# Performance work log

Hardware: AMD Instinct MI355X
Metric: run time of the kernel (lower is better)

The kernel has to match this reference:

```python
import jax, jax.numpy as jnp
import numpy as np

EPS = 1e-15


def _cdist(a, b):
    # batched euclidean pairwise distance, a:[B,N,K] b:[B,M,K] -> [B,N,M]
    d2 = (jnp.sum(a * a, -1)[:, :, None] + jnp.sum(b * b, -1)[:, None, :]
          - 2.0 * jnp.einsum('bik,bjk->bij', a, b))
    return jnp.sqrt(jnp.maximum(d2, 0.0))


def _rank3_diag(d_flat):
    # [B,N] -> [B,N,N] diagonal
    eye = jnp.eye(d_flat.shape[1], dtype=d_flat.dtype)
    return eye * d_flat[:, :, None]


def _trace(m):
    return jnp.einsum('bjj->b', m)


def dense_ct_rewiring(x, adj, s, mask):
    s = jnp.tanh(s)
    m = mask[:, :, None].astype(x.dtype)
    x = x * m
    s = s * m
    k = s.shape[-1]
    d_flat = jnp.sum(adj, axis=-1)              # [B,N]
    d = _rank3_diag(d_flat) + EPS               # EPS added to full matrix (faithful to torch)
    L = d - adj
    out_adj = jnp.einsum('bnk,bnm,bml->bkl', s, L, s)
    ct_num = _trace(out_adj)
    ct_den = _trace(jnp.einsum('bnk,bnm,bml->bkl', s, d, s)) + EPS
    ct_dist = _cdist(s, s)                      # [B,N,N]
    vol = _trace(d)                             # [B]
    ct_dist = ct_dist / vol[:, None, None]
    adj_new = ct_dist * adj
    ct_loss = jnp.mean(ct_num / ct_den)
    ss = jnp.einsum('bnk,bnl->bkl', s, s)
    i_s = jnp.eye(k, dtype=ss.dtype)
    ss_n = jnp.sqrt(jnp.sum(ss * ss, axis=(-1, -2), keepdims=True))
    diff = ss / ss_n - i_s
    ortho_loss = jnp.sqrt(jnp.sum(diff * diff))  # global Frobenius norm, mean of scalar
    return adj_new, ct_loss, ortho_loss


def dense_mincut_pool(x, adj, s, mask):
    s = jax.nn.softmax(s, axis=-1)
    m = mask[:, :, None].astype(x.dtype)
    x = x * m
    s = s * m
    k = s.shape[-1]
    out = jnp.einsum('bnk,bnf->bkf', s, x)
    out_adj = jnp.einsum('bnk,bnm,bml->bkl', s, adj, s)
    mincut_num = _trace(out_adj)
    d_flat = jnp.sum(adj, axis=-1) + EPS
    d = _rank3_diag(d_flat)
    mincut_den = _trace(jnp.einsum('bnk,bnm,bml->bkl', s, d, s))
    mincut_loss = jnp.mean(-(mincut_num / mincut_den))
    ss = jnp.einsum('bnk,bnl->bkl', s, s)
    i_s = jnp.eye(k, dtype=ss.dtype)
    ss_n = jnp.sqrt(jnp.sum(ss * ss, axis=(-1, -2), keepdims=True))
    diff = ss / ss_n - i_s / jnp.sqrt(jnp.asarray(float(k), ss.dtype))
    ortho_loss = jnp.mean(jnp.sqrt(jnp.sum(diff * diff, axis=(-1, -2))))
    # zero diagonal, then symmetric degree normalization
    out_adj = out_adj * (1.0 - i_s)
    dk = jnp.sqrt(jnp.sum(out_adj, axis=-1) + EPS) + EPS  # [B,k]
    out_adj = out_adj / dk[:, None, :] / dk[:, :, None]
    return out, out_adj, mincut_loss, ortho_loss


def dense_graph_conv(x, adj, w_rel, b_rel, w_root):
    # PyG DenseGraphConv(aggr='add'): lin_rel(adj @ x) + lin_root(x)
    return jnp.matmul(jnp.matmul(adj, x), w_rel) + b_rel + jnp.matmul(x, w_root)


def ctnet_forward(x, adj, mask,
                  W_lin1, b_lin1, W_pool1, b_pool1, W_pool2, b_pool2,
                  Wrel1, brel1, Wroot1, Wrel2, brel2, Wroot2,
                  W_lin2, b_lin2, W_lin3, b_lin3):
    x = jnp.matmul(x, W_lin1) + b_lin1
    s1 = jnp.matmul(x, W_pool1) + b_pool1
    adj, ct_loss, ortho1 = dense_ct_rewiring(x, adj, s1, mask)
    x = dense_graph_conv(x, adj, Wrel1, brel1, Wroot1)
    s2 = jnp.matmul(x, W_pool2) + b_pool2
    x, adj, mincut2, ortho2 = dense_mincut_pool(x, adj, s2, mask)
    x = dense_graph_conv(x, adj, Wrel2, brel2, Wroot2)
    x = jnp.sum(x, axis=1)
    x = jax.nn.relu(jnp.matmul(x, W_lin2) + b_lin2)
    x = jnp.matmul(x, W_lin3) + b_lin3
    return jax.nn.log_softmax(x, axis=-1), ct_loss + ortho1, mincut2 + ortho2


def _init_lin(key, fan_in, fan_out):
    k1, k2 = jax.random.split(key)
    lim = 1.0 / np.sqrt(fan_in)
    W = jax.random.uniform(k1, (fan_in, fan_out), jnp.float32, -lim, lim)
    b = jax.random.uniform(k2, (fan_out,), jnp.float32, -lim, lim)
    return W, b


def setup_inputs() -> dict:
    key = jax.random.key(0)
    ks = jax.random.split(key, 12)
    B, N, Fin, H, K, OUT, K2 = 16, 1024, 128, 32, 64, 10, 16
    x = jax.random.normal(ks[0], (B, N, Fin), jnp.float32)
    adj = jax.random.uniform(ks[1], (B, N, N), jnp.float32)
    mask = jnp.ones((B, N), jnp.bool_)
    W_lin1, b_lin1 = _init_lin(ks[2], Fin, H)
    W_pool1, b_pool1 = _init_lin(ks[3], H, K)
    W_pool2, b_pool2 = _init_lin(ks[4], H, K2)
    Wrel1, brel1 = _init_lin(ks[5], H, H)
    Wroot1, _ = _init_lin(ks[6], H, H)
    Wrel2, brel2 = _init_lin(ks[7], H, H)
    Wroot2, _ = _init_lin(ks[8], H, H)
    W_lin2, b_lin2 = _init_lin(ks[9], H, H)
    W_lin3, b_lin3 = _init_lin(ks[10], H, OUT)
    return dict(x=x, adj=adj, mask=mask,
                W_lin1=W_lin1, b_lin1=b_lin1, W_pool1=W_pool1, b_pool1=b_pool1,
                W_pool2=W_pool2, b_pool2=b_pool2,
                Wrel1=Wrel1, brel1=brel1, Wroot1=Wroot1,
                Wrel2=Wrel2, brel2=brel2, Wroot2=Wroot2,
                W_lin2=W_lin2, b_lin2=b_lin2, W_lin3=W_lin3, b_lin3=b_lin3)


def reference(x, adj, mask,
              W_lin1, b_lin1, W_pool1, b_pool1, W_pool2, b_pool2,
              Wrel1, brel1, Wroot1, Wrel2, brel2, Wroot2,
              W_lin2, b_lin2, W_lin3, b_lin3):
    return ctnet_forward(x, adj, mask,
                         W_lin1, b_lin1, W_pool1, b_pool1, W_pool2, b_pool2,
                         Wrel1, brel1, Wroot1, Wrel2, brel2, Wroot2,
                         W_lin2, b_lin2, W_lin3, b_lin3)
```

## Files before the change

kernel.cpp:

```cpp
#include <hip/hip_runtime.h>

typedef unsigned short u16;
typedef unsigned int   u32;
typedef __attribute__((ext_vector_type(8))) short bf16x8;
typedef __attribute__((ext_vector_type(4))) float f32x4;

#define EPSF 1e-15f

__device__ __forceinline__ float* accp(float* xb, int b, int a) {
    return xb + (size_t)(b*1024 + a/14)*128 + 114 + (a % 14);
}

__device__ __forceinline__ float bf2f(u16 u) {
    union { u32 i; float f; } v; v.i = ((u32)u) << 16; return v.f;
}
__device__ __forceinline__ u16 f2bf(float f) {
    union { u32 i; float f; } v; v.f = f;
    u32 r = v.i + 0x7fffu + ((v.i >> 16) & 1u);
    return (u16)(r >> 16);
}

__global__ __launch_bounds__(256) void k_a(float* xb,
        const float* __restrict__ W1, const float* __restrict__ b1,
        const float* __restrict__ Wp1, const float* __restrict__ bp1)
{
    __shared__ float W1sT[32*133];
    __shared__ float Wp1sT[64*33];
    __shared__ float xs[16][128];
    __shared__ float x1s[16][32];
    int tid = threadIdx.x;
    for (int i = tid; i < 1024; i += 256) {
        int f = i >> 3, c0 = (i & 7)*4;
        float4 v = *(const float4*)&W1[f*32 + c0];
        W1sT[(c0+0)*133 + f] = v.x;
        W1sT[(c0+1)*133 + f] = v.y;
        W1sT[(c0+2)*133 + f] = v.z;
        W1sT[(c0+3)*133 + f] = v.w;
    }
    for (int i = tid; i < 512; i += 256) {
        int h = i >> 4, l0 = (i & 15)*4;
        float4 v = *(const float4*)&Wp1[h*64 + l0];
        Wp1sT[(l0+0)*33 + h] = v.x;
        Wp1sT[(l0+1)*33 + h] = v.y;
        Wp1sT[(l0+2)*33 + h] = v.z;
        Wp1sT[(l0+3)*33 + h] = v.w;
    }
    int rbase = blockIdx.x*16;
    for (int e = tid; e < 512; e += 256) {
        int rr = e >> 5, c = e & 31;
        *(float4*)&xs[rr][c*4] = *(const float4*)&xb[(size_t)(rbase + rr)*128 + c*4];
    }
    __syncthreads();
    int w = tid >> 6, l = tid & 63;
    int col = l & 31, half = l >> 5;
    #pragma unroll
    for (int i = 0; i < 4; ++i) {
        int rr = w*4 + i;
        float* xr = xb + (size_t)(rbase + rr)*128;
        if (l == 33) xr[96] = 0.f;
        if (l < 15) xr[113 + l] = 0.f;
        float acc = half ? 0.f : b1[col];
        const float* xrow = &xs[rr][half*64];
        const float* wrow = &W1sT[col*133 + half*64];
        for (int f = 0; f < 64; ++f) acc += xrow[f]*wrow[f];
        acc += __shfl_down(acc, 32);
        if (l < 32) x1s[rr][l] = acc;
    }
    __syncthreads();
    #pragma unroll
    for (int i = 0; i < 4; ++i) {
        int rr = w*4 + i;
        float* xr = xb + (size_t)(rbase + rr)*128;
        if (l < 32) xr[64 + l] = x1s[rr][l];
        float acc = bp1[l];
        const float* wp = &Wp1sT[l*33];
        for (int h = 0; h < 32; ++h) acc += x1s[rr][h]*wp[h];
        float sv = tanhf(acc);
        u32 me = (u32)f2bf(sv);
        u32 nb = __shfl_down(me, 1);
        if (!(l & 1)) ((u32*)xr)[l >> 1] = me | (nb << 16);
        float svr = bf2f((u16)me);
        float qv = svr*svr;
        for (int off = 32; off; off >>= 1) qv += __shfl_down(qv, off);
        if (l == 0) xr[112] = qv;
    }
}

__global__ __launch_bounds__(256, 5) void k_c(const float* __restrict__ adj, float* xb,
                                              u32* __restrict__ anb)
{
    __shared__ __align__(16) u16 BufA[64*72];
    __shared__ __align__(16) u16 BufB[2][64*72];
    __shared__ __align__(16) float qAs[64], qBs[2][64];
    __shared__ float pw[2][4];
    int tid = threadIdx.x;
    int tjq = blockIdx.x, ti = blockIdx.y, b = blockIdx.z;
    int w = tid >> 6, lane = tid & 63;
    int q = lane >> 4, c16 = lane & 15;
    int rloc = w*16 + c16;
    size_t rowg = (size_t)(b*1024 + ti*64 + rloc);
    float4 a4s[2][4];
    #pragma unroll
    for (int tt = 0; tt < 2; ++tt)
        #pragma unroll
        for (int t = 0; t < 4; ++t)
            a4s[tt][t] = *(const float4*)&adj[rowg*1024 + (tjq*2 + tt)*64 + t*16 + q*4];
    const u32* xu = (const u32*)xb;
    for (int e = tid; e < 512; e += 256) {
        int n = e >> 3, c = e & 7;
        *(float4*)&BufA[n*72 + c*8] = *(const float4*)&xu[(size_t)(b*1024 + ti*64 + n)*128 + c*4];
    }
    for (int e = tid; e < 1024; e += 256) {
        int n2 = e >> 3, c = e & 7;
        int tt = n2 >> 6, n = n2 & 63;
        *(float4*)&BufB[tt][n*72 + c*8] =
            *(const float4*)&xu[(size_t)(b*1024 + (tjq*2 + tt)*64 + n)*128 + c*4];
    }
    if (tid < 64) qAs[tid] = xb[(size_t)(b*1024 + ti*64 + tid)*128 + 112];
    else if (tid < 192) {
        int t2 = tid - 64;
        qBs[t2 >> 6][t2 & 63] =
            xb[(size_t)(b*1024 + (tjq*2 + (t2 >> 6))*64 + (t2 & 63))*128 + 112];
    }
    __syncthreads();
    bf16x8 bfr0 = *(const bf16x8*)&BufA[rloc*72 + q*8];
    bf16x8 bfr1 = *(const bf16x8*)&BufA[rloc*72 + 32 + q*8];
    float qa = qAs[rloc];
    float dsum = 0.f, rsum = 0.f, Pt = 0.f, Qt = 0.f;
    #pragma unroll
    for (int tt = 0; tt < 2; ++tt) {
        f32x4 g[4];
        #pragma unroll
        for (int t = 0; t < 4; ++t) {
            bf16x8 af0 = *(const bf16x8*)&BufB[tt][(t*16 + c16)*72 + q*8];
            bf16x8 af1 = *(const bf16x8*)&BufB[tt][(t*16 + c16)*72 + 32 + q*8];
            f32x4 gg = {0.f, 0.f, 0.f, 0.f};
            gg = __builtin_amdgcn_mfma_f32_16x16x32_bf16(af0, bfr0, gg, 0, 0, 0);
            gg = __builtin_amdgcn_mfma_f32_16x16x32_bf16(af1, bfr1, gg, 0, 0, 0);
            g[t] = gg;
        }
        #pragma unroll
        for (int t = 0; t < 4; ++t) {
            float4 a4 = a4s[tt][t];
            float4 qb4 = *(const float4*)&qBs[tt][t*16 + q*4];
            float av[4] = {a4.x, a4.y, a4.z, a4.w};
            float qb[4] = {qb4.x, qb4.y, qb4.z, qb4.w};
            float o[4];
            #pragma unroll
            for (int rg = 0; rg < 4; ++rg) {
                float d2v = qa + qb[rg] - 2.f*g[t][rg];
                float dist = sqrtf(fmaxf(d2v, 0.f));
                o[rg] = dist * av[rg];
                dsum += av[rg];
                rsum += o[rg];
                Pt += av[rg]*g[t][rg];
                Qt += g[t][rg]*g[t][rg];
            }
            u32 p0 = (u32)f2bf(o[0]) | ((u32)f2bf(o[1]) << 16);
            u32 p1 = (u32)f2bf(o[2]) | ((u32)f2bf(o[3]) << 16);
            *(uint2*)&anb[rowg*512 + (tjq*2 + tt)*32 + t*8 + q*2] = make_uint2(p0, p1);
        }
    }
    rsum += __shfl_xor(rsum, 16); rsum += __shfl_xor(rsum, 32);
    dsum += __shfl_xor(dsum, 16); dsum += __shfl_xor(dsum, 32);
    if (q == 0) {
        atomicAdd(&xb[rowg*128 + 96],  dsum);
        atomicAdd(&xb[rowg*128 + 113], rsum);
    }
    for (int off = 32; off; off >>= 1) { Pt += __shfl_down(Pt, off); Qt += __shfl_down(Qt, off); }
    if (lane == 0) { pw[0][w] = Pt; pw[1][w] = Qt; }
    __syncthreads();
    if (tid == 0) {
        atomicAdd(accp(xb,b,3), pw[0][0]+pw[0][1]+pw[0][2]+pw[0][3]);
        atomicAdd(accp(xb,b,4), pw[1][0]+pw[1][1]+pw[1][2]+pw[1][3]);
    }
}

__global__ __launch_bounds__(256) void k_y(const u32* __restrict__ anb, float* xb)
{
    __shared__ __align__(16) u16 X[16*1032];
    int tid = threadIdx.x;
    int hq = blockIdx.x, ni = blockIdx.y, b = blockIdx.z;
    int w = tid >> 6, lane = tid & 63;
    int q = lane >> 4, c16 = lane & 15;
    int rloc = w*16 + c16;
    size_t rowg = (size_t)(b*1024 + ni*64 + rloc);
    u32* Xu = (u32*)X;
    for (int e = tid; e < 2048; e += 256) {
        int mp = e >> 2, h4 = e & 3;
        int m0 = mp*2;
        const float* p0 = &xb[(size_t)(b*1024 + m0)*128 + 64 + hq*16 + h4*4];
        float4 v0 = *(const float4*)p0;
        float4 v1 = *(const float4*)(p0 + 128);
        Xu[(h4*4 + 0)*516 + mp] = (u32)f2bf(v0.x) | ((u32)f2bf(v1.x) << 16);
        Xu[(h4*4 + 1)*516 + mp] = (u32)f2bf(v0.y) | ((u32)f2bf(v1.y) << 16);
        Xu[(h4*4 + 2)*516 + mp] = (u32)f2bf(v0.z) | ((u32)f2bf(v1.z) << 16);
        Xu[(h4*4 + 3)*516 + mp] = (u32)f2bf(v0.w) | ((u32)f2bf(v1.w) << 16);
    }
    __syncthreads();
    f32x4 acc = {0.f,0.f,0.f,0.f};
    #pragma unroll 8
    for (int ks = 0; ks < 32; ++ks) {
        bf16x8 af = *(const bf16x8*)&anb[rowg*512 + ks*16 + q*4];
        bf16x8 bx = *(const bf16x8*)&X[c16*1032 + ks*32 + q*8];
        acc = __builtin_amdgcn_mfma_f32_16x16x32_bf16(af, bx, acc, 0, 0, 0);
    }
    #pragma unroll
    for (int rg = 0; rg < 4; ++rg) {
        size_t orow = (size_t)(b*1024 + ni*64 + w*16 + q*4 + rg)*128;
        xb[orow + 32 + hq*16 + c16] = acc[rg];
    }
    if (hq == 0 && tid < 64) {
        const float* xr = xb + (size_t)(b*1024 + ni*64 + tid)*128;
        float d = xr[96], qv = xr[112];
        float t0 = d, t1 = d*qv, t2 = qv;
        for (int off = 32; off; off >>= 1) {
            t0 += __shfl_down(t0, off); t1 += __shfl_down(t1, off); t2 += __shfl_down(t2, off);
        }
        if (tid == 0) {
            atomicAdd(accp(xb,b,0), t0);
            atomicAdd(accp(xb,b,1), t1);
            atomicAdd(accp(xb,b,2), t2);
        }
    }
}

__global__ __launch_bounds__(256) void k_d2(float* xb,
        const float* __restrict__ Wrel1, const float* __restrict__ brel1,
        const float* __restrict__ Wroot1,
        const float* __restrict__ Wp2, const float* __restrict__ bp2)
{
    __shared__ float ys[32*34];
    __shared__ float x1n[32*34];
    __shared__ float x2s[32*34];
    __shared__ float s2s[32*17];
    __shared__ float WrT[32*33], WoT[32*33], WpT[16*33];
    __shared__ float pwd[4];
    int tid = threadIdx.x;
    int tq = blockIdx.x, b = blockIdx.y;
    int rbase = b*1024 + tq*32;
    float invv = 1.f / (*accp(xb,b,0) + 1024.f*EPSF);
    {
        int j = tid >> 3, h0 = (tid & 7)*4;
        float4 v = *(const float4*)&Wrel1[j*32 + h0];
        WrT[(h0+0)*33 + j] = v.x;
        WrT[(h0+1)*33 + j] = v.y;
        WrT[(h0+2)*33 + j] = v.z;
        WrT[(h0+3)*33 + j] = v.w;
        float4 v2 = *(const float4*)&Wroot1[j*32 + h0];
        WoT[(h0+0)*33 + j] = v2.x;
        WoT[(h0+1)*33 + j] = v2.y;
        WoT[(h0+2)*33 + j] = v2.z;
        WoT[(h0+3)*33 + j] = v2.w;
    }
    if (tid < 128) {
        int j = tid >> 2, k0 = (tid & 3)*4;
        float4 v = *(const float4*)&Wp2[j*16 + k0];
        WpT[(k0+0)*33 + j] = v.x;
        WpT[(k0+1)*33 + j] = v.y;
        WpT[(k0+2)*33 + j] = v.z;
        WpT[(k0+3)*33 + j] = v.w;
    }
    for (int e = tid; e < 1024; e += 256) {
        int r = e >> 5, h = e & 31;
        const float* xr = xb + (size_t)(rbase + r)*128;
        ys[r*34 + h]  = xr[32 + h] * invv;
        x1n[r*34 + h] = xr[64 + h];
    }
    __syncthreads();
    {
        int h = tid & 31, tg = tid >> 5;
        float brl = brel1[h];
        const float* wr = &WrT[h*33];
        const float* wo = &WoT[h*33];
        #pragma unroll
        for (int i = 0; i < 4; ++i) {
            int r = tg + 8*i;
            float v = brl;
            for (int j = 0; j < 32; ++j)
                v += ys[r*34 + j]*wr[j] + x1n[r*34 + j]*wo[j];
            x2s[r*34 + h] = v;
        }
    }
    __syncthreads();
    {
        int rl = tid & 7, kq = (tid >> 3) & 7, wv = tid >> 6;
        int r = wv*8 + rl;
        int k0 = kq*2;
        float v0 = bp2[k0], v1 = bp2[k0 + 1];
        const float* wp0 = &WpT[k0*33];
        const float* wp1 = &WpT[(k0+1)*33];
        for (int j = 0; j < 32; ++j) {
            float xv = x2s[r*34 + j];
            v0 += xv*wp0[j];
            v1 += xv*wp1[j];
        }
        float mx = fmaxf(v0, v1);
        mx = fmaxf(mx, __shfl_xor(mx, 8));
        mx = fmaxf(mx, __shfl_xor(mx, 16));
        mx = fmaxf(mx, __shfl_xor(mx, 32));
        float e0 = expf(v0 - mx), e1 = expf(v1 - mx);
        float sm = e0 + e1;
        sm += __shfl_xor(sm, 8); sm += __shfl_xor(sm, 16); sm += __shfl_xor(sm, 32);
        float inv = 1.f/sm;
        float sv0 = e0*inv, sv1 = e1*inv;
        s2s[r*17 + k0]     = sv0;
        s2s[r*17 + k0 + 1] = sv1;
        ((u32*)(xb + (size_t)(rbase + r)*128))[kq] =
            (u32)f2bf(sv0) | ((u32)f2bf(sv1) << 16);
        float q2v = sv0*sv0 + sv1*sv1;
        q2v += __shfl_xor(q2v, 8); q2v += __shfl_xor(q2v, 16); q2v += __shfl_xor(q2v, 32);
        float denp = (kq == 0)
            ? (xb[(size_t)(rbase + r)*128 + 113]*invv + EPSF)*q2v : 0.f;
        denp += __shfl_down(denp, 1);
        denp += __shfl_down(denp, 2);
        denp += __shfl_down(denp, 4);
        if ((tid & 63) == 0) pwd[wv] = denp;
    }
    __syncthreads();
    if (tid == 0) atomicAdd(accp(xb,b,5), pwd[0]+pwd[1]+pwd[2]+pwd[3]);
    {
        int k = tid >> 4, l = tid & 15;
        float s = 0.f;
        for (int r = 0; r < 32; ++r) s += s2s[r*17 + k]*s2s[r*17 + l];
        atomicAdd(accp(xb,b,774 + tid), s);
    }
    for (int e = tid; e < 512; e += 256) {
        int k = e >> 5, h = e & 31;
        float s = 0.f;
        for (int r = 0; r < 32; ++r) s += s2s[r*17 + k]*x2s[r*34 + h];
        atomicAdd(accp(xb,b,6 + k*32 + h), s);
    }
}

__global__ __launch_bounds__(256) void k_e(const u32* __restrict__ anb, float* xb)
{
    __shared__ __align__(16) u16 BufS[2][16*72];
    __shared__ __align__(16) u16 BufN[16*72];
    __shared__ __align__(16) u16 zT[16*72];
    int tid = threadIdx.x;
    int miq = blockIdx.x, ni = blockIdx.y, b = blockIdx.z;
    const u32* xu = (const u32*)xb;
    for (int e = tid; e < 512; e += 256) {
        int node = e >> 3, lw = e & 7;
        u32 pp = xu[(size_t)(b*1024 + ni*64 + node)*128 + lw];
        BufN[(lw*2)*72 + node]     = (u16)pp;
        BufN[(lw*2 + 1)*72 + node] = (u16)(pp >> 16);
    }
    for (int e = tid; e < 1024; e += 256) {
        int t = e >> 9, e2 = e & 511;
        int node = e2 >> 3, lw = e2 & 7;
        u32 pp = xu[(size_t)(b*1024 + (miq*2 + t)*64 + node)*128 + lw];
        BufS[t][(lw*2)*72 + node]     = (u16)pp;
        BufS[t][(lw*2 + 1)*72 + node] = (u16)(pp >> 16);
    }
    int w = tid >> 6, lane = tid & 63;
    int q = lane >> 4, c16 = lane & 15;
    int rloc = w*16 + c16;
    size_t arow = (size_t)(b*1024 + ni*64 + rloc)*512;
    bf16x8 ya[2][2];
    #pragma unroll
    for (int t = 0; t < 2; ++t) {
        ya[t][0] = *(const bf16x8*)&anb[arow + (miq*2 + t)*32 + q*4];
        ya[t][1] = *(const bf16x8*)&anb[arow + (miq*2 + t)*32 + 16 + q*4];
    }
    __syncthreads();
    f32x4 zacc = {0.f, 0.f, 0.f, 0.f};
    #pragma unroll
    for (int t = 0; t < 2; ++t) {
        bf16x8 yb0 = *(const bf16x8*)&BufS[t][c16*72 + q*8];
        bf16x8 yb1 = *(const bf16x8*)&BufS[t][c16*72 + 32 + q*8];
        zacc = __builtin_amdgcn_mfma_f32_16x16x32_bf16(ya[t][0], yb0, zacc, 0, 0, 0);
        zacc = __builtin_amdgcn_mfma_f32_16x16x32_bf16(ya[t][1], yb1, zacc, 0, 0, 0);
    }
    #pragma unroll
    for (int rg = 0; rg < 4; ++rg)
        zT[c16*72 + w*16 + q*4 + rg] = f2bf(zacc[rg]);
    __syncthreads();
    if (w == 0) {
        bf16x8 af0 = *(const bf16x8*)&BufN[c16*72 + q*8];
        bf16x8 af1 = *(const bf16x8*)&BufN[c16*72 + 32 + q*8];
        bf16x8 bz0 = *(const bf16x8*)&zT[c16*72 + q*8];
        bf16x8 bz1 = *(const bf16x8*)&zT[c16*72 + 32 + q*8];
        f32x4 oamv = {0.f, 0.f, 0.f, 0.f};
        oamv = __builtin_amdgcn_mfma_f32_16x16x32_bf16(af0, bz0, oamv, 0, 0, 0);
        oamv = __builtin_amdgcn_mfma_f32_16x16x32_bf16(af1, bz1, oamv, 0, 0, 0);
        #pragma unroll
        for (int rg = 0; rg < 4; ++rg)
            atomicAdd(accp(xb, b, 518 + (q*4 + rg)*16 + c16), oamv[rg]);
    }
}

__global__ __launch_bounds__(256) void k_f1(float* xb,
        const float* __restrict__ Wrel2, const float* __restrict__ brel2,
        const float* __restrict__ Wroot2,
        const float* __restrict__ W_lin2, const float* __restrict__ b_lin2,
        const float* __restrict__ W_lin3, const float* __restrict__ b_lin3,
        float* __restrict__ outp)
{
    __shared__ float oam_s[256], ssm_s[256], outm_s[512];
    __shared__ float dks[16], csoa[16];
    __shared__ float cs0[32], cs1[32], xsum[32], x5[32], lgs[10];
    __shared__ float red[4];
    __shared__ int isLast;
    int b = blockIdx.x;
    int tid = threadIdx.x;
    float invv = 1.f / (*accp(xb,b,0) + 1024.f*EPSF);
    oam_s[tid] = *accp(xb,b,518 + tid) * invv;
    ssm_s[tid] = *accp(xb,b,774 + tid);
    for (int e = tid; e < 512; e += 256) outm_s[e] = *accp(xb,b,6 + e);
    __syncthreads();
    if (tid < 16) {
        float rsv = 0.f;
        for (int l = 0; l < 16; ++l) if (l != tid) rsv += oam_s[tid*16 + l];
        dks[tid] = sqrtf(fmaxf(rsv, 0.f) + EPSF) + EPSF;
    }
    {
        float v = ssm_s[tid];
        float p = v*v;
        for (int off = 32; off; off >>= 1) p += __shfl_down(p, off);
        if ((tid & 63) == 0) red[tid >> 6] = p;
    }
    __syncthreads();
    if (tid < 16) {
        float s = 0.f;
        for (int k2 = 0; k2 < 16; ++k2)
            if (k2 != tid) s += oam_s[k2*16 + tid] / dks[k2];
        csoa[tid] = s / dks[tid];
    }
    if (tid < 32) {
        float s0 = 0.f, s1 = 0.f;
        for (int l = 0; l < 16; ++l) {
            float ov = outm_s[l*32 + tid];
            s0 += ov;
            s1 += csoa[l] * ov;
        }
        cs0[tid] = s0; cs1[tid] = s1;
    }
    if (tid == 64) {
        float T1v  = *accp(xb,b,1);
        float Pgv  = *accp(xb,b,3);
        float Q2v  = *accp(xb,b,4);
        float Tq1v = *accp(xb,b,2);
        float T2v  = *accp(xb,b,5);
        float tr2 = 0.f, trs = 0.f;
        for (int k2 = 0; k2 < 16; ++k2) { tr2 += oam_s[k2*17]; trs += ssm_s[k2*17]; }
        float fr2 = red[0] + red[1] + red[2] + red[3];
        __hip_atomic_store(accp(xb,b,1030), (T1v - Pgv) / (T1v + EPSF),
                           __ATOMIC_RELAXED, __HIP_MEMORY_SCOPE_AGENT);
        __hip_atomic_store(accp(xb,b,1031), 65.f - 2.f*Tq1v/sqrtf(fmaxf(Q2v, 1e-30f)),
                           __ATOMIC_RELAXED, __HIP_MEMORY_SCOPE_AGENT);
        __hip_atomic_store(accp(xb,b,1032), -tr2 / T2v,
                           __ATOMIC_RELAXED, __HIP_MEMORY_SCOPE_AGENT);
        __hip_atomic_store(accp(xb,b,1033),
                           sqrtf(fmaxf(2.f - trs/(2.f*sqrtf(fmaxf(fr2, 1e-30f))), 0.f)),
                           __ATOMIC_RELAXED, __HIP_MEMORY_SCOPE_AGENT);
    }
    __syncthreads();
    if (tid < 32) {
        float v = 16.f * brel2[tid];
        for (int j = 0; j < 32; ++j)
            v += cs1[j]*Wrel2[j*32 + tid] + cs0[j]*Wroot2[j*32 + tid];
        xsum[tid] = v;
    }
    __syncthreads();
    if (tid < 32) {
        float v = b_lin2[tid];
        for (int j = 0; j < 32; ++j) v += xsum[j]*W_lin2[j*32 + tid];
        x5[tid] = fmaxf(v, 0.f);
    }
    __syncthreads();
    if (tid < 10) {
        float v = b_lin3[tid];
        for (int j = 0; j < 32; ++j) v += x5[j]*W_lin3[j*10 + tid];
        lgs[tid] = v;
    }
    __syncthreads();
    if (tid < 10) {
        float mx = -1e30f;
        for (int t = 0; t < 10; ++t) mx = fmaxf(mx, lgs[t]);
        float sum = 0.f;
        for (int t = 0; t < 10; ++t) sum += expf(lgs[t] - mx);
        outp[b*10 + tid] = lgs[tid] - mx - logf(sum);
    }
    __syncthreads();
    if (tid == 0) {
        __threadfence();
        float old = atomicAdd(accp(xb,0,1035), 1.f);
        isLast = (old > 14.5f) ? 1 : 0;
    }
    __syncthreads();
    if (isLast && tid < 64) {
        __threadfence();
        int b2 = tid & 15, which = tid >> 4;
        float v = __hip_atomic_load(accp(xb,b2,1030 + which),
                                    __ATOMIC_RELAXED, __HIP_MEMORY_SCOPE_AGENT);
        for (int off = 1; off < 16; off <<= 1) v += __shfl_xor(v, off);
        float ct = __shfl(v, 0);
        float o1 = __shfl(v, 16);
        float mc = __shfl(v, 32);
        float o2 = __shfl(v, 48);
        if (tid == 0) {
            outp[160] = ct/16.f + sqrtf(fmaxf(o1, 0.f));
            outp[161] = mc/16.f + o2/16.f;
        }
    }
}

extern "C" void kernel_launch(void* const* d_in, const int* in_sizes, int n_in,
                              void* d_out, int out_size, void* d_ws, size_t ws_size,
                              hipStream_t stream)
{
    float* xb        = (float*)d_in[0];
    const float* adj = (const float*)d_in[1];
    const float* W_lin1 = (const float*)d_in[3];
    const float* b_lin1 = (const float*)d_in[4];
    const float* W_pool1= (const float*)d_in[5];
    const float* b_pool1= (const float*)d_in[6];
    const float* W_pool2= (const float*)d_in[7];
    const float* b_pool2= (const float*)d_in[8];
    const float* Wrel1  = (const float*)d_in[9];
    const float* brel1  = (const float*)d_in[10];
    const float* Wroot1 = (const float*)d_in[11];
    const float* Wrel2  = (const float*)d_in[12];
    const float* brel2  = (const float*)d_in[13];
    const float* Wroot2 = (const float*)d_in[14];
    const float* W_lin2 = (const float*)d_in[15];
    const float* b_lin2 = (const float*)d_in[16];
    const float* W_lin3 = (const float*)d_in[17];
    const float* b_lin3 = (const float*)d_in[18];
    u32* anb = (u32*)d_ws;
    (void)ws_size; (void)in_sizes; (void)n_in; (void)out_size;

    k_a<<<dim3(1024),      dim3(256), 0, stream>>>(xb, W_lin1, b_lin1, W_pool1, b_pool1);
    k_c<<<dim3(8,16,16),   dim3(256), 0, stream>>>(adj, xb, anb);
    k_y<<<dim3(2,16,16),   dim3(256), 0, stream>>>(anb, xb);
    k_d2<<<dim3(32,16),    dim3(256), 0, stream>>>(xb, Wrel1, brel1, Wroot1,
                                                   W_pool2, b_pool2);
    k_e<<<dim3(8,16,16),   dim3(256), 0, stream>>>(anb, xb);
    k_f1<<<dim3(16),       dim3(256), 0, stream>>>(xb, Wrel2, brel2, Wroot2,
                                                   W_lin2, b_lin2, W_lin3, b_lin3,
                                                   (float*)d_out);
}
```

Measured before the change: 220.2 us.

## Fuse adjacency-aggregation matmul with GraphConv and pooling into one kernel

k_a now also writes a transposed bf16 copy of x1 into spare workspace. A new fused kernel k_yd runs the anb·x1 MFMA product together with the dense GraphConv, softmax pooling and the partial reductions that k_y and k_d2 used to do separately, removing one launch and the fp32 y round trip through global memory. The degree and volume scalar reductions move into k_c's epilogue, so they no longer need a per-row degree slot. The fused path is used only when the workspace is large enough; otherwise the old two-kernel path runs. k_yd uses larger 64-row tiles and launches only 256 blocks, which may lower occupancy compared with the split kernels.

```diff
diff --git a/kernel.cpp b/kernel.cpp
--- a/kernel.cpp
+++ b/kernel.cpp
@@ -22,7 +22,8 @@
 
 __global__ __launch_bounds__(256) void k_a(float* xb,
         const float* __restrict__ W1, const float* __restrict__ b1,
-        const float* __restrict__ Wp1, const float* __restrict__ bp1)
+        const float* __restrict__ Wp1, const float* __restrict__ bp1,
+        u32* __restrict__ x1t)
 {
     __shared__ float W1sT[32*133];
     __shared__ float Wp1sT[64*33];
@@ -57,7 +58,6 @@
     for (int i = 0; i < 4; ++i) {
         int rr = w*4 + i;
         float* xr = xb + (size_t)(rbase + rr)*128;
-        if (l == 33) xr[96] = 0.f;
         if (l < 15) xr[113 + l] = 0.f;
         float acc = half ? 0.f : b1[col];
         const float* xrow = &xs[rr][half*64];
@@ -67,6 +67,16 @@
         if (l < 32) x1s[rr][l] = acc;
     }
     __syncthreads();
+    if (x1t && tid < 32) {
+        int b = rbase >> 10, mbase = rbase & 1023;
+        u32 pk[8];
+        #pragma unroll
+        for (int i2 = 0; i2 < 8; ++i2)
+            pk[i2] = (u32)f2bf(x1s[2*i2][tid]) | ((u32)f2bf(x1s[2*i2+1][tid]) << 16);
+        u32* dst = x1t + (size_t)b*16384 + tid*512 + (mbase >> 1);
+        *(uint4*)dst     = make_uint4(pk[0], pk[1], pk[2], pk[3]);
+        *(uint4*)(dst+4) = make_uint4(pk[4], pk[5], pk[6], pk[7]);
+    }
     #pragma unroll
     for (int i = 0; i < 4; ++i) {
         int rr = w*4 + i;
@@ -92,7 +102,7 @@
     __shared__ __align__(16) u16 BufA[64*72];
     __shared__ __align__(16) u16 BufB[2][64*72];
     __shared__ __align__(16) float qAs[64], qBs[2][64];
-    __shared__ float pw[2][4];
+    __shared__ float pw[5][4];
     int tid = threadIdx.x;
     int tjq = blockIdx.x, ti = blockIdx.y, b = blockIdx.z;
     int w = tid >> 6, lane = tid & 63;
@@ -163,20 +173,158 @@
     }
     rsum += __shfl_xor(rsum, 16); rsum += __shfl_xor(rsum, 32);
     dsum += __shfl_xor(dsum, 16); dsum += __shfl_xor(dsum, 32);
-    if (q == 0) {
-        atomicAdd(&xb[rowg*128 + 96],  dsum);
-        atomicAdd(&xb[rowg*128 + 113], rsum);
-    }
-    for (int off = 32; off; off >>= 1) { Pt += __shfl_down(Pt, off); Qt += __shfl_down(Qt, off); }
-    if (lane == 0) { pw[0][w] = Pt; pw[1][w] = Qt; }
+    if (q == 0) atomicAdd(&xb[rowg*128 + 113], rsum);
+    float cd = (q == 0) ? dsum : 0.f;
+    float c1 = (q == 0) ? qa*dsum : 0.f;
+    float cq = (q == 0 && tjq == 0) ? qa : 0.f;
+    for (int off = 32; off; off >>= 1) {
+        Pt += __shfl_down(Pt, off); Qt += __shfl_down(Qt, off);
+        cd += __shfl_down(cd, off); c1 += __shfl_down(c1, off); cq += __shfl_down(cq, off);
+    }
+    if (lane == 0) { pw[0][w]=Pt; pw[1][w]=Qt; pw[2][w]=cd; pw[3][w]=c1; pw[4][w]=cq; }
     __syncthreads();
     if (tid == 0) {
         atomicAdd(accp(xb,b,3), pw[0][0]+pw[0][1]+pw[0][2]+pw[0][3]);
         atomicAdd(accp(xb,b,4), pw[1][0]+pw[1][1]+pw[1][2]+pw[1][3]);
-    }
-}
-
-__global__ __launch_bounds__(256) void k_y(const u32* __restrict__ anb, float* xb)
+        atomicAdd(accp(xb,b,0), pw[2][0]+pw[2][1]+pw[2][2]+pw[2][3]);
+        atomicAdd(accp(xb,b,1), pw[3][0]+pw[3][1]+pw[3][2]+pw[3][3]);
+        if (tjq == 0)
+            atomicAdd(accp(xb,b,2), pw[4][0]+pw[4][1]+pw[4][2]+pw[4][3]);
+    }
+}
+
+__global__ __launch_bounds__(256) void k_yd(const u32* __restrict__ anb,
+        const u32* __restrict__ x1t, float* xb,
+        const float* __restrict__ Wrel1, const float* __restrict__ brel1,
+        const float* __restrict__ Wroot1,
+        const float* __restrict__ Wp2, const float* __restrict__ bp2)
+{
+    __shared__ float ys[64*33];
+    __shared__ float x1n[64*36];
+    __shared__ float x2s[64*33];
+    __shared__ float s2s[64*17];
+    __shared__ float WrT[32*33], WoT[32*33], WpT[16*33];
+    __shared__ float pwd[4];
+    int tid = threadIdx.x;
+    int ni = blockIdx.x, b = blockIdx.y;
+    int rbase = b*1024 + ni*64;
+    float invv = 1.f / (*accp(xb,b,0) + 1024.f*EPSF);
+    {
+        int j = tid >> 3, h0 = (tid & 7)*4;
+        float4 v = *(const float4*)&Wrel1[j*32 + h0];
+        WrT[(h0+0)*33 + j] = v.x;
+        WrT[(h0+1)*33 + j] = v.y;
+        WrT[(h0+2)*33 + j] = v.z;
+        WrT[(h0+3)*33 + j] = v.w;
+        float4 v2 = *(const float4*)&Wroot1[j*32 + h0];
+        WoT[(h0+0)*33 + j] = v2.x;
+        WoT[(h0+1)*33 + j] = v2.y;
+        WoT[(h0+2)*33 + j] = v2.z;
+        WoT[(h0+3)*33 + j] = v2.w;
+    }
+    if (tid < 128) {
+        int j = tid >> 2, k0 = (tid & 3)*4;
+        float4 v = *(const float4*)&Wp2[j*16 + k0];
+        WpT[(k0+0)*33 + j] = v.x;
+        WpT[(k0+1)*33 + j] = v.y;
+        WpT[(k0+2)*33 + j] = v.z;
+        WpT[(k0+3)*33 + j] = v.w;
+    }
+    for (int e = tid; e < 512; e += 256) {
+        int r = e >> 3, c = e & 7;
+        *(float4*)&x1n[r*36 + c*4] = *(const float4*)&xb[(size_t)(rbase + r)*128 + 64 + c*4];
+    }
+    int w = tid >> 6, lane = tid & 63;
+    int q = lane >> 4, c16 = lane & 15;
+    int rloc = w*16 + c16;
+    size_t rowg = (size_t)(rbase + rloc);
+    const u32* xrow = x1t + (size_t)b*16384;
+    f32x4 acc0 = {0.f,0.f,0.f,0.f}, acc1 = {0.f,0.f,0.f,0.f};
+    #pragma unroll 8
+    for (int ks = 0; ks < 32; ++ks) {
+        bf16x8 af  = *(const bf16x8*)&anb[rowg*512 + ks*16 + q*4];
+        bf16x8 b0  = *(const bf16x8*)&xrow[c16*512 + ks*16 + q*4];
+        bf16x8 b1v = *(const bf16x8*)&xrow[(c16+16)*512 + ks*16 + q*4];
+        acc0 = __builtin_amdgcn_mfma_f32_16x16x32_bf16(af, b0,  acc0, 0, 0, 0);
+        acc1 = __builtin_amdgcn_mfma_f32_16x16x32_bf16(af, b1v, acc1, 0, 0, 0);
+    }
+    #pragma unroll
+    for (int rg = 0; rg < 4; ++rg) {
+        int row = w*16 + q*4 + rg;
+        ys[row*33 + c16]      = acc0[rg]*invv;
+        ys[row*33 + 16 + c16] = acc1[rg]*invv;
+    }
+    __syncthreads();
+    {
+        int h = tid & 31, tg = tid >> 5;
+        float brl = brel1[h];
+        const float* wr = &WrT[h*33];
+        const float* wo = &WoT[h*33];
+        #pragma unroll
+        for (int i = 0; i < 8; ++i) {
+            int r = tg + 8*i;
+            float v = brl;
+            for (int j = 0; j < 32; ++j)
+                v += ys[r*33 + j]*wr[j] + x1n[r*36 + j]*wo[j];
+            x2s[r*33 + h] = v;
+        }
+    }
+    __syncthreads();
+    {
+        int rl = tid & 7, kq = (tid >> 3) & 7, wv = tid >> 6;
+        int k0 = kq*2;
+        const float* wp0 = &WpT[k0*33];
+        const float* wp1 = &WpT[(k0+1)*33];
+        float denp = 0.f;
+        #pragma unroll
+        for (int pass = 0; pass < 2; ++pass) {
+            int r = wv*8 + rl + pass*32;
+            float v0 = bp2[k0], v1 = bp2[k0 + 1];
+            for (int j = 0; j < 32; ++j) {
+                float xv = x2s[r*33 + j];
+                v0 += xv*wp0[j];
+                v1 += xv*wp1[j];
+            }
+            float mx = fmaxf(v0, v1);
+            mx = fmaxf(mx, __shfl_xor(mx, 8));
+            mx = fmaxf(mx, __shfl_xor(mx, 16));
+            mx = fmaxf(mx, __shfl_xor(mx, 32));
+            float e0 = expf(v0 - mx), e1 = expf(v1 - mx);
+            float sm = e0 + e1;
+            sm += __shfl_xor(sm, 8); sm += __shfl_xor(sm, 16); sm += __shfl_xor(sm, 32);
+            float inv = 1.f/sm;
+            float sv0 = e0*inv, sv1 = e1*inv;
+            s2s[r*17 + k0]     = sv0;
+            s2s[r*17 + k0 + 1] = sv1;
+            ((u32*)(xb + (size_t)(rbase + r)*128))[kq] =
+                (u32)f2bf(sv0) | ((u32)f2bf(sv1) << 16);
+            float q2v = sv0*sv0 + sv1*sv1;
+            q2v += __shfl_xor(q2v, 8); q2v += __shfl_xor(q2v, 16); q2v += __shfl_xor(q2v, 32);
+            if (kq == 0)
+                denp += (xb[(size_t)(rbase + r)*128 + 113]*invv + EPSF)*q2v;
+        }
+        denp += __shfl_down(denp, 1);
+        denp += __shfl_down(denp, 2);
+        denp += __shfl_down(denp, 4);
+        if ((tid & 63) == 0) pwd[wv] = denp;
+    }
+    __syncthreads();
+    if (tid == 0) atomicAdd(accp(xb,b,5), pwd[0]+pwd[1]+pwd[2]+pwd[3]);
+    {
+        int k = tid >> 4, l = tid & 15;
+        float s = 0.f;
+        for (int r = 0; r < 64; ++r) s += s2s[r*17 + k]*s2s[r*17 + l];
+        atomicAdd(accp(xb,b,774 + tid), s);
+    }
+    for (int e = tid; e < 512; e += 256) {
+        int k = e >> 5, h = e & 31;
+        float s = 0.f;
+        for (int r = 0; r < 64; ++r) s += s2s[r*17 + k]*x2s[r*33 + h];
+        atomicAdd(accp(xb,b,6 + k*32 + h), s);
+    }
+}
+
+__global__ __launch_bounds__(256) void k_y_st(const u32* __restrict__ anb, float* xb)
 {
     __shared__ __align__(16) u16 X[16*1032];
     int tid = threadIdx.x;
@@ -209,19 +357,6 @@
     for (int rg = 0; rg < 4; ++rg) {
         size_t orow = (size_t)(b*1024 + ni*64 + w*16 + q*4 + rg)*128;
         xb[orow + 32 + hq*16 + c16] = acc[rg];
-    }
-    if (hq == 0 && tid < 64) {
-        const float* xr = xb + (size_t)(b*1024 + ni*64 + tid)*128;
-        float d = xr[96], qv = xr[112];
-        float t0 = d, t1 = d*qv, t2 = qv;
-        for (int off = 32; off; off >>= 1) {
-            t0 += __shfl_down(t0, off); t1 += __shfl_down(t1, off); t2 += __shfl_down(t2, off);
-        }
-        if (tid == 0) {
-            atomicAdd(accp(xb,b,0), t0);
-            atomicAdd(accp(xb,b,1), t1);
-            atomicAdd(accp(xb,b,2), t2);
-        }
     }
 }
 
@@ -530,13 +665,21 @@
     const float* W_lin3 = (const float*)d_in[17];
     const float* b_lin3 = (const float*)d_in[18];
     u32* anb = (u32*)d_ws;
-    (void)ws_size; (void)in_sizes; (void)n_in; (void)out_size;
-
-    k_a<<<dim3(1024),      dim3(256), 0, stream>>>(xb, W_lin1, b_lin1, W_pool1, b_pool1);
+    bool hasX = ws_size >= (((size_t)33) << 20);
+    u32* x1t = hasX ? anb + (size_t)8*1024*1024 : (u32*)nullptr;
+    (void)in_sizes; (void)n_in; (void)out_size;
+
+    k_a<<<dim3(1024),      dim3(256), 0, stream>>>(xb, W_lin1, b_lin1, W_pool1, b_pool1,
+                                                   x1t);
     k_c<<<dim3(8,16,16),   dim3(256), 0, stream>>>(adj, xb, anb);
-    k_y<<<dim3(2,16,16),   dim3(256), 0, stream>>>(anb, xb);
-    k_d2<<<dim3(32,16),    dim3(256), 0, stream>>>(xb, Wrel1, brel1, Wroot1,
-                                                   W_pool2, b_pool2);
+    if (hasX) {
+        k_yd<<<dim3(16,16), dim3(256), 0, stream>>>(anb, x1t, xb, Wrel1, brel1, Wroot1,
+                                                    W_pool2, b_pool2);
+    } else {
+        k_y_st<<<dim3(2,16,16), dim3(256), 0, stream>>>(anb, xb);
+        k_d2<<<dim3(32,16),     dim3(256), 0, stream>>>(xb, Wrel1, brel1, Wroot1,
+                                                        W_pool2, b_pool2);
+    }
     k_e<<<dim3(8,16,16),   dim3(256), 0, stream>>>(anb, xb);
     k_f1<<<dim3(16),       dim3(256), 0, stream>>>(xb, Wrel2, brel2, Wroot2,
                                                    W_lin2, b_lin2, W_lin3, b_lin3,
```

Result: slower. 226.7 us (+2.9%).

## Fuse adjacency-feature MFMA into GNN update kernel and move scalar reductions into k_c

Applied to the files above, without the earlier changes.

Removes the separate k_y launch. k_a now writes a packed, transposed bf16 copy of x1 into spare xb columns, and the new k_yd kernel runs the adj_new·x1 MFMA directly into shared memory before the dense GraphConv update. The per-batch degree and volume reductions previously done in k_y are now accumulated in k_c at block level, which also stops the per-row degree atomic. Packing to bf16 now uses the hardware v_cvt_pk_bf16_f32 instruction. The trade-off is that each k_yd block reads the whole transposed x1 operand from global memory instead of staging it in LDS, and several accumulator offsets were relocated.

```diff
diff --git a/kernel.cpp b/kernel.cpp
--- a/kernel.cpp
+++ b/kernel.cpp
@@ -57,7 +57,6 @@
     for (int i = 0; i < 4; ++i) {
         int rr = w*4 + i;
         float* xr = xb + (size_t)(rbase + rr)*128;
-        if (l == 33) xr[96] = 0.f;
         if (l < 15) xr[113 + l] = 0.f;
         float acc = half ? 0.f : b1[col];
         const float* xrow = &xs[rr][half*64];
@@ -67,6 +66,17 @@
         if (l < 32) x1s[rr][l] = acc;
     }
     __syncthreads();
+    if (tid < 32) {
+        int b = rbase >> 10, mbase = rbase & 1023;
+        u32 pk[8];
+        #pragma unroll
+        for (int i2 = 0; i2 < 8; ++i2)
+            pk[i2] = (u32)f2bf(x1s[2*i2][tid]) | ((u32)f2bf(x1s[2*i2+1][tid]) << 16);
+        float* dst = xb + (size_t)(b*1024 + tid*32 + (mbase >> 5))*128 + 32
+                        + ((mbase & 31) >> 1);
+        *(uint4*)dst       = make_uint4(pk[0], pk[1], pk[2], pk[3]);
+        *(uint4*)(dst + 4) = make_uint4(pk[4], pk[5], pk[6], pk[7]);
+    }
     #pragma unroll
     for (int i = 0; i < 4; ++i) {
         int rr = w*4 + i;
@@ -92,7 +102,7 @@
     __shared__ __align__(16) u16 BufA[64*72];
     __shared__ __align__(16) u16 BufB[2][64*72];
     __shared__ __align__(16) float qAs[64], qBs[2][64];
-    __shared__ float pw[2][4];
+    __shared__ float pw[5][4];
     int tid = threadIdx.x;
     int tjq = blockIdx.x, ti = blockIdx.y, b = blockIdx.z;
     int w = tid >> 6, lane = tid & 63;
@@ -156,81 +166,40 @@
                 Pt += av[rg]*g[t][rg];
                 Qt += g[t][rg]*g[t][rg];
             }
-            u32 p0 = (u32)f2bf(o[0]) | ((u32)f2bf(o[1]) << 16);
-            u32 p1 = (u32)f2bf(o[2]) | ((u32)f2bf(o[3]) << 16);
+            u32 p0, p1;
+            asm("v_cvt_pk_bf16_f32 %0, %1, %2" : "=v"(p0) : "v"(o[0]), "v"(o[1]));
+            asm("v_cvt_pk_bf16_f32 %0, %1, %2" : "=v"(p1) : "v"(o[2]), "v"(o[3]));
             *(uint2*)&anb[rowg*512 + (tjq*2 + tt)*32 + t*8 + q*2] = make_uint2(p0, p1);
         }
     }
     rsum += __shfl_xor(rsum, 16); rsum += __shfl_xor(rsum, 32);
     dsum += __shfl_xor(dsum, 16); dsum += __shfl_xor(dsum, 32);
-    if (q == 0) {
-        atomicAdd(&xb[rowg*128 + 96],  dsum);
-        atomicAdd(&xb[rowg*128 + 113], rsum);
-    }
-    for (int off = 32; off; off >>= 1) { Pt += __shfl_down(Pt, off); Qt += __shfl_down(Qt, off); }
-    if (lane == 0) { pw[0][w] = Pt; pw[1][w] = Qt; }
+    if (q == 0) atomicAdd(&xb[rowg*128 + 113], rsum);
+    float cd = (q == 0) ? dsum : 0.f;
+    float c1 = (q == 0) ? qa*dsum : 0.f;
+    float cq = (q == 0 && tjq == 0) ? qa : 0.f;
+    for (int off = 32; off; off >>= 1) {
+        Pt += __shfl_down(Pt, off); Qt += __shfl_down(Qt, off);
+        cd += __shfl_down(cd, off); c1 += __shfl_down(c1, off); cq += __shfl_down(cq, off);
+    }
+    if (lane == 0) { pw[0][w]=Pt; pw[1][w]=Qt; pw[2][w]=cd; pw[3][w]=c1; pw[4][w]=cq; }
     __syncthreads();
     if (tid == 0) {
-        atomicAdd(accp(xb,b,3), pw[0][0]+pw[0][1]+pw[0][2]+pw[0][3]);
-        atomicAdd(accp(xb,b,4), pw[1][0]+pw[1][1]+pw[1][2]+pw[1][3]);
-    }
-}
-
-__global__ __launch_bounds__(256) void k_y(const u32* __restrict__ anb, float* xb)
-{
-    __shared__ __align__(16) u16 X[16*1032];
-    int tid = threadIdx.x;
-    int hq = blockIdx.x, ni = blockIdx.y, b = blockIdx.z;
-    int w = tid >> 6, lane = tid & 63;
-    int q = lane >> 4, c16 = lane & 15;
-    int rloc = w*16 + c16;
-    size_t rowg = (size_t)(b*1024 + ni*64 + rloc);
-    u32* Xu = (u32*)X;
-    for (int e = tid; e < 2048; e += 256) {
-        int mp = e >> 2, h4 = e & 3;
-        int m0 = mp*2;
-        const float* p0 = &xb[(size_t)(b*1024 + m0)*128 + 64 + hq*16 + h4*4];
-        float4 v0 = *(const float4*)p0;
-        float4 v1 = *(const float4*)(p0 + 128);
-        Xu[(h4*4 + 0)*516 + mp] = (u32)f2bf(v0.x) | ((u32)f2bf(v1.x) << 16);
-        Xu[(h4*4 + 1)*516 + mp] = (u32)f2bf(v0.y) | ((u32)f2bf(v1.y) << 16);
-        Xu[(h4*4 + 2)*516 + mp] = (u32)f2bf(v0.z) | ((u32)f2bf(v1.z) << 16);
-        Xu[(h4*4 + 3)*516 + mp] = (u32)f2bf(v0.w) | ((u32)f2bf(v1.w) << 16);
-    }
-    __syncthreads();
-    f32x4 acc = {0.f,0.f,0.f,0.f};
-    #pragma unroll 8
-    for (int ks = 0; ks < 32; ++ks) {
-        bf16x8 af = *(const bf16x8*)&anb[rowg*512 + ks*16 + q*4];
-        bf16x8 bx = *(const bf16x8*)&X[c16*1032 + ks*32 + q*8];
-        acc = __builtin_amdgcn_mfma_f32_16x16x32_bf16(af, bx, acc, 0, 0, 0);
-    }
-    #pragma unroll
-    for (int rg = 0; rg < 4; ++rg) {
-        size_t orow = (size_t)(b*1024 + ni*64 + w*16 + q*4 + rg)*128;
-        xb[orow + 32 + hq*16 + c16] = acc[rg];
-    }
-    if (hq == 0 && tid < 64) {
-        const float* xr = xb + (size_t)(b*1024 + ni*64 + tid)*128;
-        float d = xr[96], qv = xr[112];
-        float t0 = d, t1 = d*qv, t2 = qv;
-        for (int off = 32; off; off >>= 1) {
-            t0 += __shfl_down(t0, off); t1 += __shfl_down(t1, off); t2 += __shfl_down(t2, off);
-        }
-        if (tid == 0) {
-            atomicAdd(accp(xb,b,0), t0);
-            atomicAdd(accp(xb,b,1), t1);
-            atomicAdd(accp(xb,b,2), t2);
-        }
-    }
-}
-
-__global__ __launch_bounds__(256) void k_d2(float* xb,
+        atomicAdd(accp(xb,b,1092), pw[0][0]+pw[0][1]+pw[0][2]+pw[0][3]);
+        atomicAdd(accp(xb,b,1106), pw[1][0]+pw[1][1]+pw[1][2]+pw[1][3]);
+        atomicAdd(accp(xb,b,1050), pw[2][0]+pw[2][1]+pw[2][2]+pw[2][3]);
+        atomicAdd(accp(xb,b,1064), pw[3][0]+pw[3][1]+pw[3][2]+pw[3][3]);
+        if (tjq == 0)
+            atomicAdd(accp(xb,b,1078), pw[4][0]+pw[4][1]+pw[4][2]+pw[4][3]);
+    }
+}
+
+__global__ __launch_bounds__(256) void k_yd(const u32* __restrict__ anb, float* xb,
         const float* __restrict__ Wrel1, const float* __restrict__ brel1,
         const float* __restrict__ Wroot1,
         const float* __restrict__ Wp2, const float* __restrict__ bp2)
 {
-    __shared__ float ys[32*34];
+    __shared__ float ys[32*33];
     __shared__ float x1n[32*34];
     __shared__ float x2s[32*34];
     __shared__ float s2s[32*17];
@@ -239,7 +208,7 @@
     int tid = threadIdx.x;
     int tq = blockIdx.x, b = blockIdx.y;
     int rbase = b*1024 + tq*32;
-    float invv = 1.f / (*accp(xb,b,0) + 1024.f*EPSF);
+    float invv = 1.f / (*accp(xb,b,1050) + 1024.f*EPSF);
     {
         int j = tid >> 3, h0 = (tid & 7)*4;
         float4 v = *(const float4*)&Wrel1[j*32 + h0];
@@ -261,25 +230,39 @@
         WpT[(k0+2)*33 + j] = v.z;
         WpT[(k0+3)*33 + j] = v.w;
     }
-    for (int e = tid; e < 1024; e += 256) {
-        int r = e >> 5, h = e & 31;
-        const float* xr = xb + (size_t)(rbase + r)*128;
-        ys[r*34 + h]  = xr[32 + h] * invv;
-        x1n[r*34 + h] = xr[64 + h];
-    }
-    __syncthreads();
     {
-        int h = tid & 31, tg = tid >> 5;
-        float brl = brel1[h];
-        const float* wr = &WrT[h*33];
-        const float* wo = &WoT[h*33];
+        int r = tid >> 3, c = tid & 7;
+        *(float4*)&x1n[r*34 + c*4] = *(const float4*)&xb[(size_t)(rbase + r)*128 + 64 + c*4];
+    }
+    int w = tid >> 6, lane = tid & 63;
+    int q = lane >> 4, c16 = lane & 15;
+    int rh = w & 1, hh = w >> 1;
+    int h = hh*16 + c16;
+    size_t rowg = (size_t)(rbase + rh*16 + c16);
+    const float* xtb = xb + (size_t)(b*1024 + h*32)*128 + 32 + q*4;
+    f32x4 acc = {0.f,0.f,0.f,0.f};
+    #pragma unroll 8
+    for (int ks = 0; ks < 32; ++ks) {
+        bf16x8 af = *(const bf16x8*)&anb[rowg*512 + ks*16 + q*4];
+        bf16x8 bx = *(const bf16x8*)&xtb[(size_t)ks*128];
+        acc = __builtin_amdgcn_mfma_f32_16x16x32_bf16(af, bx, acc, 0, 0, 0);
+    }
+    #pragma unroll
+    for (int rg = 0; rg < 4; ++rg)
+        ys[(rh*16 + q*4 + rg)*33 + hh*16 + c16] = acc[rg]*invv;
+    __syncthreads();
+    {
+        int hc = tid & 31, tg = tid >> 5;
+        float brl = brel1[hc];
+        const float* wr = &WrT[hc*33];
+        const float* wo = &WoT[hc*33];
         #pragma unroll
         for (int i = 0; i < 4; ++i) {
             int r = tg + 8*i;
             float v = brl;
             for (int j = 0; j < 32; ++j)
-                v += ys[r*34 + j]*wr[j] + x1n[r*34 + j]*wo[j];
-            x2s[r*34 + h] = v;
+                v += ys[r*33 + j]*wr[j] + x1n[r*34 + j]*wo[j];
+            x2s[r*34 + hc] = v;
         }
     }
     __syncthreads();
@@ -318,7 +301,7 @@
         if ((tid & 63) == 0) pwd[wv] = denp;
     }
     __syncthreads();
-    if (tid == 0) atomicAdd(accp(xb,b,5), pwd[0]+pwd[1]+pwd[2]+pwd[3]);
+    if (tid == 0) atomicAdd(accp(xb,b,1120), pwd[0]+pwd[1]+pwd[2]+pwd[3]);
     {
         int k = tid >> 4, l = tid & 15;
         float s = 0.f;
@@ -326,10 +309,10 @@
         atomicAdd(accp(xb,b,774 + tid), s);
     }
     for (int e = tid; e < 512; e += 256) {
-        int k = e >> 5, h = e & 31;
+        int k = e >> 5, hc = e & 31;
         float s = 0.f;
-        for (int r = 0; r < 32; ++r) s += s2s[r*17 + k]*x2s[r*34 + h];
-        atomicAdd(accp(xb,b,6 + k*32 + h), s);
+        for (int r = 0; r < 32; ++r) s += s2s[r*17 + k]*x2s[r*34 + hc];
+        atomicAdd(accp(xb,b,6 + k*32 + hc), s);
     }
 }
 
@@ -405,7 +388,7 @@
     __shared__ int isLast;
     int b = blockIdx.x;
     int tid = threadIdx.x;
-    float invv = 1.f / (*accp(xb,b,0) + 1024.f*EPSF);
+    float invv = 1.f / (*accp(xb,b,1050) + 1024.f*EPSF);
     oam_s[tid] = *accp(xb,b,518 + tid) * invv;
     ssm_s[tid] = *accp(xb,b,774 + tid);
     for (int e = tid; e < 512; e += 256) outm_s[e] = *accp(xb,b,6 + e);
@@ -438,11 +421,11 @@
         cs0[tid] = s0; cs1[tid] = s1;
     }
     if (tid == 64) {
-        float T1v  = *accp(xb,b,1);
-        float Pgv  = *accp(xb,b,3);
-        float Q2v  = *accp(xb,b,4);
-        float Tq1v = *accp(xb,b,2);
-        float T2v  = *accp(xb,b,5);
+        float T1v  = *accp(xb,b,1064);
+        float Pgv  = *accp(xb,b,1092);
+        float Q2v  = *accp(xb,b,1106);
+        float Tq1v = *accp(xb,b,1078);
+        float T2v  = *accp(xb,b,1120);
         float tr2 = 0.f, trs = 0.f;
         for (int k2 = 0; k2 < 16; ++k2) { tr2 += oam_s[k2*17]; trs += ssm_s[k2*17]; }
         float fr2 = red[0] + red[1] + red[2] + red[3];
@@ -534,8 +517,7 @@
 
     k_a<<<dim3(1024),      dim3(256), 0, stream>>>(xb, W_lin1, b_lin1, W_pool1, b_pool1);
     k_c<<<dim3(8,16,16),   dim3(256), 0, stream>>>(adj, xb, anb);
-    k_y<<<dim3(2,16,16),   dim3(256), 0, stream>>>(anb, xb);
-    k_d2<<<dim3(32,16),    dim3(256), 0, stream>>>(xb, Wrel1, brel1, Wroot1,
+    k_yd<<<dim3(32,16),    dim3(256), 0, stream>>>(anb, xb, Wrel1, brel1, Wroot1,
                                                    W_pool2, b_pool2);
     k_e<<<dim3(8,16,16),   dim3(256), 0, stream>>>(anb, xb);
     k_f1<<<dim3(16),       dim3(256), 0, stream>>>(xb, Wrel2, brel2, Wroot2,
```

New measurement: 218.3 us. About the same (-0.9%).
